# Optimization experiments

Hardware: AMD Instinct MI355X
Metric: run time of the kernel (lower is better)

Reference implementation:

```python
import jax, jax.numpy as jnp
import numpy as np

N_NODES = 100000
N_EDGES = 1250000
D_IN, D_HID, D_OUT = 64, 64, 64


def _sage_conv(x, edge_index, W_l, b_l, W_r, num_nodes):
    # PyG SAGEConv (aggr='mean', root_weight=True):
    #   out_i = W_l @ mean_{j->i} x_j + b_l + W_r @ x_i
    src, dst = edge_index[0], edge_index[1]
    msgs = x[src]  # [E, D] gather
    agg = jax.ops.segment_sum(msgs, dst, num_segments=num_nodes)  # [N, D]
    cnt = jax.ops.segment_sum(jnp.ones((src.shape[0],), x.dtype), dst,
                              num_segments=num_nodes)
    mean = agg / jnp.maximum(cnt, 1.0)[:, None]
    return mean @ W_l.T + b_l + x @ W_r.T


def setup_inputs() -> dict:
    key = jax.random.key(0)
    ks = jax.random.split(key, 8)
    s_in = 1.0 / np.sqrt(D_IN)
    s_hid = 1.0 / np.sqrt(D_HID)
    return {
        "x": jax.random.normal(ks[0], (N_NODES, D_IN), jnp.float32),
        "edge_index": jax.random.randint(ks[1], (2, N_EDGES), 0, N_NODES, jnp.int32),
        "W1_l": jax.random.normal(ks[2], (D_HID, D_IN), jnp.float32) * s_in,
        "b1": jnp.zeros((D_HID,), jnp.float32),
        "W1_r": jax.random.normal(ks[3], (D_HID, D_IN), jnp.float32) * s_in,
        "W2_l": jax.random.normal(ks[4], (D_OUT, D_HID), jnp.float32) * s_hid,
        "b2": jnp.zeros((D_OUT,), jnp.float32),
        "W2_r": jax.random.normal(ks[5], (D_OUT, D_HID), jnp.float32) * s_hid,
    }


def reference(x, edge_index, W1_l, b1, W1_r, W2_l, b2, W2_r):
    n = x.shape[0]
    h = _sage_conv(x, edge_index, W1_l, b1, W1_r, n)
    h = jax.nn.relu(h)
    # F.dropout(p=0.1, training=self.training): identity in eval mode
    out = _sage_conv(h, edge_index, W2_l, b2, W2_r, n)
    return out
```

## Files before the change

### kernel.cpp

```cpp
#include <hip/hip_runtime.h>

#define D 64
#define CAP 4096
#define CHUNK 4096
#define CASTB 512
#define MROW_STRIDE 72

typedef unsigned int u32;
typedef unsigned short u16;
typedef unsigned char u8;
typedef __attribute__((ext_vector_type(8))) short bf16x8_t;
typedef __attribute__((ext_vector_type(4))) float f32x4_t;
typedef __attribute__((ext_vector_type(2))) float f32x2_t;

__device__ __forceinline__ u16 f2b(float f) {
  u32 u = __float_as_uint(f);
  u += 0x7FFFu + ((u >> 16) & 1u);
  return (u16)(u >> 16);
}
__device__ __forceinline__ float hi2f(u32 u) { return __uint_as_float(u & 0xFFFF0000u); }
__device__ __forceinline__ float lo2f(u32 u) { return __uint_as_float(u << 16); }

__launch_bounds__(512)
__global__ void k_init(const float* __restrict__ W1l, const float* __restrict__ W1r,
                       const float* __restrict__ W2l, const float* __restrict__ W2r,
                       u16* __restrict__ Bp1, u16* __restrict__ Bp2,
                       int* __restrict__ bcur, int* __restrict__ rowptr,
                       int n, int nE, int nb) {
  int b = blockIdx.x;
  int t = threadIdx.x;
  if (b == 2) {
    for (int i = t; i < nb; i += 512) bcur[i] = i * CAP;
    if (t == 0) rowptr[n] = nE;
    return;
  }
  const float* Wl = b ? W2l : W1l;
  const float* Wr = b ? W2r : W1r;
  u16* Bp = b ? Bp2 : Bp1;
  for (int idx = t; idx < 8192; idx += 512) {
    int j = idx & 7;
    int lane = (idx >> 3) & 63;
    int st = idx >> 9;
    int s = st >> 2, tt = st & 3;
    int k = s * 32 + ((lane >> 4) << 3) + j;
    int c = tt * 16 + (lane & 15);
    float v = (k < 64) ? Wl[c * 64 + k] : Wr[c * 64 + (k - 64)];
    Bp[idx] = f2b(v);
  }
}

__launch_bounds__(512)
__global__ void k_bin(const int* __restrict__ src, const int* __restrict__ dst,
                      int* __restrict__ bcur, u32* __restrict__ ebuf, int nE, int nb,
                      int eblocks, const float* __restrict__ x,
                      u16* __restrict__ xb, u8* __restrict__ x8, int total8) {
  __shared__ int hist[512];
  __shared__ int excl[512];
  __shared__ int lcur[512];
  __shared__ int gstart[512];
  __shared__ u32 ent[CHUNK];
  __shared__ u16 ebkt[CHUNK];

  int t = threadIdx.x;
  if ((int)blockIdx.x >= eblocks) {
    int cb = blockIdx.x - eblocks;
    for (int i = cb * 512 + t; i < total8; i += CASTB * 512) {
      const float4* p = (const float4*)(x + (size_t)i * 8);
      float4 v0 = p[0], v1 = p[1];
      uint4 w;
      w.x = (u32)f2b(v0.x) | ((u32)f2b(v0.y) << 16);
      w.y = (u32)f2b(v0.z) | ((u32)f2b(v0.w) << 16);
      w.z = (u32)f2b(v1.x) | ((u32)f2b(v1.y) << 16);
      w.w = (u32)f2b(v1.z) | ((u32)f2b(v1.w) << 16);
      *(uint4*)(xb + (size_t)i * 8) = w;
      u32 a8 = __builtin_amdgcn_cvt_pk_fp8_f32(v0.x, v0.y, 0, false);
      a8 = __builtin_amdgcn_cvt_pk_fp8_f32(v0.z, v0.w, a8, true);
      u32 b8 = __builtin_amdgcn_cvt_pk_fp8_f32(v1.x, v1.y, 0, false);
      b8 = __builtin_amdgcn_cvt_pk_fp8_f32(v1.z, v1.w, b8, true);
      uint2 w8; w8.x = a8; w8.y = b8;
      *(uint2*)(x8 + (size_t)i * 8) = w8;
    }
    return;
  }

  int base = blockIdx.x * CHUNK;
  int cnt = nE - base; if (cnt > CHUNK) cnt = CHUNK;

  hist[t] = 0;
  __syncthreads();

  int ls[8], ld[8];
  #pragma unroll
  for (int k = 0; k < 8; ++k) {
    int i = t + k * 512;
    if (i < cnt) {
      ls[k] = src[base + i];
      ld[k] = dst[base + i];
      atomicAdd(&hist[ld[k] >> 8], 1);
    } else ls[k] = -1;
  }
  __syncthreads();

  int bcnt = hist[t];
  for (int off = 1; off < 512; off <<= 1) {
    int u = (t >= off) ? hist[t - off] : 0;
    __syncthreads();
    hist[t] += u;
    __syncthreads();
  }
  int ex = hist[t] - bcnt;
  excl[t] = ex;
  lcur[t] = ex;
  if (t < nb && bcnt > 0) gstart[t] = atomicAdd(&bcur[t], bcnt);
  __syncthreads();

  #pragma unroll
  for (int k = 0; k < 8; ++k) {
    if (ls[k] >= 0) {
      int b = ld[k] >> 8;
      int p = atomicAdd(&lcur[b], 1);
      ent[p]  = ((u32)ls[k] << 8) | (u32)(ld[k] & 255);
      ebkt[p] = (u16)b;
    }
  }
  __syncthreads();

  for (int i = t; i < cnt; i += 512) {
    int b = ebkt[i];
    ebuf[gstart[b] + (i - excl[b])] = ent[i];
  }
}

__launch_bounds__(256)
__global__ void k_build(const u32* __restrict__ ebuf, const int* __restrict__ bcur,
                        int* __restrict__ rowptr, int* __restrict__ csr, int n) {
  __shared__ int hist[256];
  __shared__ int lcur[256];
  __shared__ int sbase;
  int b = blockIdx.x;
  int t = threadIdx.x;
  int base_s = b * CAP;
  int cnt = bcur[b] - base_s;

  int ps = 0;
  for (int i = t; i < b; i += 256) ps += bcur[i] - i * CAP;
  hist[t] = ps;
  __syncthreads();
  for (int off = 128; off > 0; off >>= 1) {
    if (t < off) hist[t] += hist[t + off];
    __syncthreads();
  }
  if (t == 0) sbase = hist[0];
  __syncthreads();
  int base_d = sbase;

  hist[t] = 0;
  __syncthreads();
  for (int i = t; i < cnt; i += 256)
    atomicAdd(&hist[ebuf[base_s + i] & 255], 1);
  __syncthreads();

  int v = hist[t];
  int node = b * 256 + t;
  for (int off = 1; off < 256; off <<= 1) {
    int u = (t >= off) ? hist[t - off] : 0;
    __syncthreads();
    hist[t] += u;
    __syncthreads();
  }
  int ex = hist[t] - v;
  if (node < n) rowptr[node] = base_d + ex;
  lcur[t] = ex;
  __syncthreads();

  for (int i = t; i < cnt; i += 256) {
    u32 e = ebuf[base_s + i];
    int p = atomicAdd(&lcur[e & 255], 1);
    csr[base_d + p] = (int)(e >> 8);
  }
}

__launch_bounds__(256)
__global__ void k_gd(const int* __restrict__ rowptr, const int* __restrict__ csr,
                     const u8* __restrict__ gin8, const u16* __restrict__ xin,
                     const u16* __restrict__ Bp, const float* __restrict__ bias,
                     u16* __restrict__ out_bf, u8* __restrict__ out8,
                     float* __restrict__ out_f32, int n, int do_relu) {
  __shared__ int idx_s[4][4][64];
  __shared__ u16 mrow[16 * MROW_STRIDE];

  int tid = threadIdx.x;
  int wave = tid >> 6;
  int lane = tid & 63;
  int g = lane >> 4;
  int q = lane & 15;
  int node0 = blockIdx.x * 16;
  int local = wave * 4 + g;
  int node = node0 + local;

  int rs = rowptr[node];
  int re = rowptr[node + 1];

  f32x2_t acc01 = {0.f, 0.f}, acc23 = {0.f, 0.f};
  for (int cb = rs; cb < re; cb += 64) {
    int mcnt = re - cb; if (mcnt > 64) mcnt = 64;
    #pragma unroll
    for (int k = 0; k < 4; ++k) {
      int sidx = k * 16 + q;
      if (sidx < mcnt) idx_s[wave][g][sidx] = csr[cb + sidx];
    }
    int j = 0;
    for (; j + 8 <= mcnt; j += 8) {
      u32 v[8];
      #pragma unroll
      for (int k = 0; k < 8; ++k) {
        int i0 = idx_s[wave][g][j + k];
        v[k] = *(const u32*)(gin8 + (size_t)i0 * D + q * 4);
      }
      #pragma unroll
      for (int k = 0; k < 8; ++k) {
        acc01 += __builtin_amdgcn_cvt_pk_f32_fp8(v[k], false);
        acc23 += __builtin_amdgcn_cvt_pk_f32_fp8(v[k], true);
      }
    }
    for (; j + 4 <= mcnt; j += 4) {
      u32 v[4];
      #pragma unroll
      for (int k = 0; k < 4; ++k) {
        int i0 = idx_s[wave][g][j + k];
        v[k] = *(const u32*)(gin8 + (size_t)i0 * D + q * 4);
      }
      #pragma unroll
      for (int k = 0; k < 4; ++k) {
        acc01 += __builtin_amdgcn_cvt_pk_f32_fp8(v[k], false);
        acc23 += __builtin_amdgcn_cvt_pk_f32_fp8(v[k], true);
      }
    }
    for (; j < mcnt; ++j) {
      int i0 = idx_s[wave][g][j];
      u32 v0 = *(const u32*)(gin8 + (size_t)i0 * D + q * 4);
      acc01 += __builtin_amdgcn_cvt_pk_f32_fp8(v0, false);
      acc23 += __builtin_amdgcn_cvt_pk_f32_fp8(v0, true);
    }
  }

  float inv = 1.0f / fmaxf((float)(re - rs), 1.0f);
  uint2 w;
  w.x = (u32)f2b(acc01.x * inv) | ((u32)f2b(acc01.y * inv) << 16);
  w.y = (u32)f2b(acc23.x * inv) | ((u32)f2b(acc23.y * inv) << 16);
  *(uint2*)(mrow + local * MROW_STRIDE + q * 4) = w;
  __syncthreads();

  const bf16x8_t* Bp8 = (const bf16x8_t*)Bp;
  int arow = node0 + (lane & 15);
  const bf16x8_t* xr8 = (const bf16x8_t*)(xin + (size_t)arow * D);
  int ko = lane >> 4;

  f32x4_t acc = {};
  #pragma unroll
  for (int s = 0; s < 4; ++s) {
    bf16x8_t a;
    if (s < 2) a = *(const bf16x8_t*)(mrow + (lane & 15) * MROW_STRIDE + s * 32 + ko * 8);
    else       a = xr8[(s - 2) * 4 + ko];
    bf16x8_t b = Bp8[(s * 4 + wave) * 64 + lane];
    acc = __builtin_amdgcn_mfma_f32_16x16x32_bf16(a, b, acc, 0, 0, 0);
  }

  int f = wave * 16 + (lane & 15);
  float bv = bias[f];
  int r0 = (lane >> 4) * 4;
  #pragma unroll
  for (int r = 0; r < 4; ++r) {
    int row = node0 + r0 + r;
    float v = acc[r] + bv;
    if (do_relu) v = fmaxf(v, 0.f);
    if (out_bf) {
      out_bf[(size_t)row * D + f] = f2b(v);
      u32 p8 = __builtin_amdgcn_cvt_pk_fp8_f32(v, 0.f, 0, false);
      out8[(size_t)row * D + f] = (u8)(p8 & 0xFFu);
    } else {
      out_f32[(size_t)row * D + f] = v;
    }
  }
}

extern "C" void kernel_launch(void* const* d_in, const int* in_sizes, int n_in,
                              void* d_out, int out_size, void* d_ws, size_t ws_size,
                              hipStream_t stream) {
  const float* x   = (const float*)d_in[0];
  const int*   ei  = (const int*)d_in[1];
  const float* W1l = (const float*)d_in[2];
  const float* b1  = (const float*)d_in[3];
  const float* W1r = (const float*)d_in[4];
  const float* W2l = (const float*)d_in[5];
  const float* b2  = (const float*)d_in[6];
  const float* W2r = (const float*)d_in[7];

  int n  = in_sizes[0] / D;
  int nE = in_sizes[1] / 2;
  const int* src = ei;
  const int* dst = ei + nE;
  int nb = (n + 255) / 256;

  char* w = (char*)d_ws;
  auto alloc = [&](size_t bytes) { char* p = w; w += (bytes + 255) & ~(size_t)255; return p; };
  int* bcur   = (int*)alloc((size_t)nb * 4);
  int* rowptr = (int*)alloc((size_t)(n + 1) * 4);
  int* csr    = (int*)alloc((size_t)nE * 4);
  u16* xb     = (u16*)alloc((size_t)n * D * 2);
  u8*  x8     = (u8*) alloc((size_t)n * D);
  u8*  h8     = (u8*) alloc((size_t)n * D);
  size_t hbytes = (size_t)n * D * 2;
  size_t ebytes = (size_t)nb * CAP * 4;
  char* hov   = alloc(hbytes > ebytes ? hbytes : ebytes);
  u32* ebuf   = (u32*)hov;
  u16* hb     = (u16*)hov;
  u16* Bp1    = (u16*)alloc(8192 * 2);
  u16* Bp2    = (u16*)alloc(8192 * 2);

  int eblocks = (nE + CHUNK - 1) / CHUNK;
  int gdblocks = n / 16;

  k_init <<<3,               512, 0, stream>>>(W1l, W1r, W2l, W2r, Bp1, Bp2,
                                               bcur, rowptr, n, nE, nb);
  k_bin  <<<eblocks + CASTB, 512, 0, stream>>>(src, dst, bcur, ebuf, nE, nb,
                                               eblocks, x, xb, x8, n * D / 8);
  k_build<<<nb,              256, 0, stream>>>(ebuf, bcur, rowptr, csr, n);

  k_gd<<<gdblocks, 256, 0, stream>>>(rowptr, csr, x8, xb, Bp1, b1,
                                     hb, h8, nullptr, n, 1);
  k_gd<<<gdblocks, 256, 0, stream>>>(rowptr, csr, h8, hb, Bp2, b2,
                                     nullptr, nullptr, (float*)d_out, n, 0);
}
```

Before: 99.87 us.

## Split fp8 feature tables into two 32-byte halves and gather each separately

Stores the fp8 node features as two separate tables holding features 0-31 and 32-63, so each row becomes 32 bytes. The aggregation kernel now makes two passes over the neighbor list, one per half, with each lane loading 2 bytes instead of 4. The aim is a smaller per-pass working set so gathered rows hit in cache more often. In exchange it doubles the csr index reads and the number of gather instructions, and each lane now issues narrower loads.

Measured after the change: 122.5 us. 22.7% more time.

```diff
diff --git a/kernel.cpp b/kernel.cpp
--- a/kernel.cpp
+++ b/kernel.cpp
@@ -18,8 +18,6 @@
   u += 0x7FFFu + ((u >> 16) & 1u);
   return (u16)(u >> 16);
 }
-__device__ __forceinline__ float hi2f(u32 u) { return __uint_as_float(u & 0xFFFF0000u); }
-__device__ __forceinline__ float lo2f(u32 u) { return __uint_as_float(u << 16); }
 
 __launch_bounds__(512)
 __global__ void k_init(const float* __restrict__ W1l, const float* __restrict__ W1r,
@@ -53,7 +51,8 @@
 __global__ void k_bin(const int* __restrict__ src, const int* __restrict__ dst,
                       int* __restrict__ bcur, u32* __restrict__ ebuf, int nE, int nb,
                       int eblocks, const float* __restrict__ x,
-                      u16* __restrict__ xb, u8* __restrict__ x8, int total8) {
+                      u16* __restrict__ xb, u8* __restrict__ x8lo,
+                      u8* __restrict__ x8hi, int total8) {
   __shared__ int hist[512];
   __shared__ int excl[512];
   __shared__ int lcur[512];
@@ -78,7 +77,11 @@
       u32 b8 = __builtin_amdgcn_cvt_pk_fp8_f32(v1.x, v1.y, 0, false);
       b8 = __builtin_amdgcn_cvt_pk_fp8_f32(v1.z, v1.w, b8, true);
       uint2 w8; w8.x = a8; w8.y = b8;
-      *(uint2*)(x8 + (size_t)i * 8) = w8;
+      int node = i >> 3;
+      int f0 = (i & 7) * 8;
+      u8* dstp = (f0 < 32) ? (x8lo + (size_t)node * 32 + f0)
+                           : (x8hi + (size_t)node * 32 + (f0 - 32));
+      *(uint2*)dstp = w8;
     }
     return;
   }
@@ -182,10 +185,12 @@
 
 __launch_bounds__(256)
 __global__ void k_gd(const int* __restrict__ rowptr, const int* __restrict__ csr,
-                     const u8* __restrict__ gin8, const u16* __restrict__ xin,
+                     const u8* __restrict__ g8lo, const u8* __restrict__ g8hi,
+                     const u16* __restrict__ xin,
                      const u16* __restrict__ Bp, const float* __restrict__ bias,
-                     u16* __restrict__ out_bf, u8* __restrict__ out8,
-                     float* __restrict__ out_f32, int n, int do_relu) {
+                     u16* __restrict__ out_bf, u8* __restrict__ out8lo,
+                     u8* __restrict__ out8hi, float* __restrict__ out_f32,
+                     int n, int do_relu) {
   __shared__ int idx_s[4][4][64];
   __shared__ u16 mrow[16 * MROW_STRIDE];
 
@@ -200,55 +205,51 @@
 
   int rs = rowptr[node];
   int re = rowptr[node + 1];
-
-  f32x2_t acc01 = {0.f, 0.f}, acc23 = {0.f, 0.f};
-  for (int cb = rs; cb < re; cb += 64) {
-    int mcnt = re - cb; if (mcnt > 64) mcnt = 64;
-    #pragma unroll
-    for (int k = 0; k < 4; ++k) {
-      int sidx = k * 16 + q;
-      if (sidx < mcnt) idx_s[wave][g][sidx] = csr[cb + sidx];
-    }
-    int j = 0;
-    for (; j + 8 <= mcnt; j += 8) {
-      u32 v[8];
+  float inv = 1.0f / fmaxf((float)(re - rs), 1.0f);
+
+  #pragma unroll
+  for (int p = 0; p < 2; ++p) {
+    const u8* gt = p ? g8hi : g8lo;
+    f32x2_t acc = {0.f, 0.f};
+    for (int cb = rs; cb < re; cb += 64) {
+      int mcnt = re - cb; if (mcnt > 64) mcnt = 64;
       #pragma unroll
-      for (int k = 0; k < 8; ++k) {
-        int i0 = idx_s[wave][g][j + k];
-        v[k] = *(const u32*)(gin8 + (size_t)i0 * D + q * 4);
+      for (int k = 0; k < 4; ++k) {
+        int sidx = k * 16 + q;
+        if (sidx < mcnt) idx_s[wave][g][sidx] = csr[cb + sidx];
       }
-      #pragma unroll
-      for (int k = 0; k < 8; ++k) {
-        acc01 += __builtin_amdgcn_cvt_pk_f32_fp8(v[k], false);
-        acc23 += __builtin_amdgcn_cvt_pk_f32_fp8(v[k], true);
+      int j = 0;
+      for (; j + 8 <= mcnt; j += 8) {
+        u16 v[8];
+        #pragma unroll
+        for (int k = 0; k < 8; ++k) {
+          int i0 = idx_s[wave][g][j + k];
+          v[k] = *(const u16*)(gt + (size_t)i0 * 32 + q * 2);
+        }
+        #pragma unroll
+        for (int k = 0; k < 8; ++k)
+          acc += __builtin_amdgcn_cvt_pk_f32_fp8((u32)v[k], false);
+      }
+      for (; j + 4 <= mcnt; j += 4) {
+        u16 v[4];
+        #pragma unroll
+        for (int k = 0; k < 4; ++k) {
+          int i0 = idx_s[wave][g][j + k];
+          v[k] = *(const u16*)(gt + (size_t)i0 * 32 + q * 2);
+        }
+        #pragma unroll
+        for (int k = 0; k < 4; ++k)
+          acc += __builtin_amdgcn_cvt_pk_f32_fp8((u32)v[k], false);
+      }
+      for (; j < mcnt; ++j) {
+        int i0 = idx_s[wave][g][j];
+        u16 v0 = *(const u16*)(gt + (size_t)i0 * 32 + q * 2);
+        acc += __builtin_amdgcn_cvt_pk_f32_fp8((u32)v0, false);
       }
     }
-    for (; j + 4 <= mcnt; j += 4) {
-      u32 v[4];
-      #pragma unroll
-      for (int k = 0; k < 4; ++k) {
-        int i0 = idx_s[wave][g][j + k];
-        v[k] = *(const u32*)(gin8 + (size_t)i0 * D + q * 4);
-      }
-      #pragma unroll
-      for (int k = 0; k < 4; ++k) {
-        acc01 += __builtin_amdgcn_cvt_pk_f32_fp8(v[k], false);
-        acc23 += __builtin_amdgcn_cvt_pk_f32_fp8(v[k], true);
-      }
-    }
-    for (; j < mcnt; ++j) {
-      int i0 = idx_s[wave][g][j];
-      u32 v0 = *(const u32*)(gin8 + (size_t)i0 * D + q * 4);
-      acc01 += __builtin_amdgcn_cvt_pk_f32_fp8(v0, false);
-      acc23 += __builtin_amdgcn_cvt_pk_f32_fp8(v0, true);
-    }
-  }
-
-  float inv = 1.0f / fmaxf((float)(re - rs), 1.0f);
-  uint2 w;
-  w.x = (u32)f2b(acc01.x * inv) | ((u32)f2b(acc01.y * inv) << 16);
-  w.y = (u32)f2b(acc23.x * inv) | ((u32)f2b(acc23.y * inv) << 16);
-  *(uint2*)(mrow + local * MROW_STRIDE + q * 4) = w;
+    u32 wv = (u32)f2b(acc.x * inv) | ((u32)f2b(acc.y * inv) << 16);
+    *(u32*)(mrow + local * MROW_STRIDE + p * 32 + q * 2) = wv;
+  }
   __syncthreads();
 
   const bf16x8_t* Bp8 = (const bf16x8_t*)Bp;
@@ -277,7 +278,9 @@
     if (out_bf) {
       out_bf[(size_t)row * D + f] = f2b(v);
       u32 p8 = __builtin_amdgcn_cvt_pk_fp8_f32(v, 0.f, 0, false);
-      out8[(size_t)row * D + f] = (u8)(p8 & 0xFFu);
+      u8 byte = (u8)(p8 & 0xFFu);
+      if (f < 32) out8lo[(size_t)row * 32 + f] = byte;
+      else        out8hi[(size_t)row * 32 + (f - 32)] = byte;
     } else {
       out_f32[(size_t)row * D + f] = v;
     }
@@ -308,8 +311,10 @@
   int* rowptr = (int*)alloc((size_t)(n + 1) * 4);
   int* csr    = (int*)alloc((size_t)nE * 4);
   u16* xb     = (u16*)alloc((size_t)n * D * 2);
-  u8*  x8     = (u8*) alloc((size_t)n * D);
-  u8*  h8     = (u8*) alloc((size_t)n * D);
+  u8*  x8lo   = (u8*) alloc((size_t)n * 32);
+  u8*  x8hi   = (u8*) alloc((size_t)n * 32);
+  u8*  h8lo   = (u8*) alloc((size_t)n * 32);
+  u8*  h8hi   = (u8*) alloc((size_t)n * 32);
   size_t hbytes = (size_t)n * D * 2;
   size_t ebytes = (size_t)nb * CAP * 4;
   char* hov   = alloc(hbytes > ebytes ? hbytes : ebytes);
@@ -324,11 +329,12 @@
   k_init <<<3,               512, 0, stream>>>(W1l, W1r, W2l, W2r, Bp1, Bp2,
                                                bcur, rowptr, n, nE, nb);
   k_bin  <<<eblocks + CASTB, 512, 0, stream>>>(src, dst, bcur, ebuf, nE, nb,
-                                               eblocks, x, xb, x8, n * D / 8);
+                                               eblocks, x, xb, x8lo, x8hi,
+                                               n * D / 8);
   k_build<<<nb,              256, 0, stream>>>(ebuf, bcur, rowptr, csr, n);
 
-  k_gd<<<gdblocks, 256, 0, stream>>>(rowptr, csr, x8, xb, Bp1, b1,
-                                     hb, h8, nullptr, n, 1);
-  k_gd<<<gdblocks, 256, 0, stream>>>(rowptr, csr, h8, hb, Bp2, b2,
-                                     nullptr, nullptr, (float*)d_out, n, 0);
-}
+  k_gd<<<gdblocks, 256, 0, stream>>>(rowptr, csr, x8lo, x8hi, xb, Bp1, b1,
+                                     hb, h8lo, h8hi, nullptr, n, 1);
+  k_gd<<<gdblocks, 256, 0, stream>>>(rowptr, csr, h8lo, h8hi, hb, Bp2, b2,
+                                     nullptr, nullptr, nullptr, (float*)d_out, n, 0);
+}
```
